# Performance work log

Hardware: AMD Instinct MI355X
Metric: run time of the kernel (lower is better)

## Reference

```python
import jax, jax.numpy as jnp
import numpy as np

DIM = 192
HEADS = 6
WS = 8
SHIFT = 4
POS_DIM = 12  # (dim//4)//4
HIDDEN = 768
EPS = 1e-5


def _win_partition(x, ws):
    B, H, W, C = x.shape
    x = x.reshape(B, H // ws, ws, W // ws, ws, C)
    return x.transpose(0, 1, 3, 2, 4, 5).reshape(-1, ws, ws, C)


def _win_reverse(w, ws, H, W):
    B = w.shape[0] // ((H // ws) * (W // ws))
    x = w.reshape(B, H // ws, W // ws, ws, ws, -1)
    return x.transpose(0, 1, 3, 2, 4, 5).reshape(B, H, W, -1)


def _calc_mask(H, W, ws, shift):
    img = np.zeros((1, H, W, 1), np.float32)
    sl = (slice(0, -ws), slice(-ws, -shift), slice(-shift, None))
    cnt = 0
    for hs in sl:
        for wsl in sl:
            img[:, hs, wsl, :] = cnt
            cnt += 1
    mw = img.reshape(1, H // ws, ws, W // ws, ws, 1).transpose(0, 1, 3, 2, 4, 5).reshape(-1, ws * ws)
    am = mw[:, None, :] - mw[:, :, None]
    am = np.where(am != 0, -100.0, 0.0).astype(np.float32)
    return am  # [nW, N, N]


def _rel_index(ws):
    coords = np.stack(np.meshgrid(np.arange(ws), np.arange(ws), indexing='ij')).reshape(2, -1)
    rel = (coords[:, :, None] - coords[:, None, :]).transpose(1, 2, 0)
    rel[..., 0] += ws - 1
    rel[..., 1] += ws - 1
    rel[..., 0] *= 2 * ws - 1
    return rel.sum(-1)  # [N, N]


def _biases(ws):
    bh = np.arange(1 - ws, ws)
    bw = np.arange(1 - ws, ws)
    b = np.stack(np.meshgrid(bh, bw, indexing='ij')).reshape(2, -1).T
    return b.astype(np.float32)  # [(2ws-1)^2, 2]


def _ln(x, g, b):
    mu = jnp.mean(x, -1, keepdims=True)
    var = jnp.var(x, -1, keepdims=True)
    return (x - mu) / jnp.sqrt(var + EPS) * g + b


def setup_inputs() -> dict:
    key = jax.random.key(0)
    ks = jax.random.split(key, 20)
    B, L, C = 8, 128 * 128, DIM
    d = {
        'x': jax.random.normal(ks[0], (B, L, C), jnp.float32),
        'k_v': jnp.zeros((1,), jnp.float32),
        'H': 128, 'W': 128,
        'n1_g': jnp.ones((C,)), 'n1_b': jnp.zeros((C,)),
        'qkv_w': jax.random.normal(ks[1], (C, 3 * C)) * 0.02,
        'qkv_b': jnp.zeros((3 * C,)),
        'proj_w': jax.random.normal(ks[2], (C, C)) * 0.02,
        'proj_b': jnp.zeros((C,)),
        'pp_w': jax.random.normal(ks[3], (2, POS_DIM)) * 0.02,
        'pp_b': jnp.zeros((POS_DIM,)),
        'p1_g': jnp.ones((POS_DIM,)), 'p1_b': jnp.zeros((POS_DIM,)),
        'p1_w': jax.random.normal(ks[4], (POS_DIM, POS_DIM)) * 0.02,
        'p1_bias': jnp.zeros((POS_DIM,)),
        'p2_g': jnp.ones((POS_DIM,)), 'p2_b': jnp.zeros((POS_DIM,)),
        'p2_w': jax.random.normal(ks[5], (POS_DIM, POS_DIM)) * 0.02,
        'p2_bias': jnp.zeros((POS_DIM,)),
        'p3_g': jnp.ones((POS_DIM,)), 'p3_b': jnp.zeros((POS_DIM,)),
        'p3_w': jax.random.normal(ks[6], (POS_DIM, HEADS)) * 0.02,
        'p3_bias': jnp.zeros((HEADS,)),
        'n2_g': jnp.ones((C,)), 'n2_b': jnp.zeros((C,)),
        'fc1_w': jax.random.normal(ks[7], (C, HIDDEN)) * 0.02,
        'fc1_b': jnp.zeros((HIDDEN,)),
        'fc2_w': jax.random.normal(ks[8], (HIDDEN, C)) * 0.02,
        'fc2_b': jnp.zeros((C,)),
    }
    return d


def reference(x, k_v, H, W, n1_g, n1_b, qkv_w, qkv_b, proj_w, proj_b,
              pp_w, pp_b, p1_g, p1_b, p1_w, p1_bias, p2_g, p2_b, p2_w, p2_bias,
              p3_g, p3_b, p3_w, p3_bias, n2_g, n2_b, fc1_w, fc1_b, fc2_w, fc2_b):
    B, L, C = x.shape
    N = WS * WS
    hd = C // HEADS
    scale = hd ** (-0.5)

    rel_idx = jnp.asarray(_rel_index(WS).reshape(-1))            # [N*N]
    biases = jnp.asarray(_biases(WS))                            # [(2WS-1)^2, 2]
    mask = jnp.asarray(_calc_mask(H, W, WS, SHIFT))              # [nW, N, N]

    shortcut = x
    h = _ln(x, n1_g, n1_b).reshape(B, H, W, C)
    h = jnp.roll(h, (-SHIFT, -SHIFT), (1, 2))
    xw = _win_partition(h, WS).reshape(-1, N, C)                 # [B*nW, N, C]
    B_ = xw.shape[0]

    qkv = (xw @ qkv_w + qkv_b).reshape(B_, N, 3, HEADS, hd).transpose(2, 0, 3, 1, 4)
    q, k, v = qkv[0] * scale, qkv[1], qkv[2]                     # [B_, H, N, hd]
    attn = jnp.einsum('bhnd,bhmd->bhnm', q, k)

    # dynamic position bias MLP (residual=False path)
    pos = biases @ pp_w + pp_b
    pos = jax.nn.relu(_ln(pos, p1_g, p1_b)) @ p1_w + p1_bias
    pos = jax.nn.relu(_ln(pos, p2_g, p2_b)) @ p2_w + p2_bias
    pos = jax.nn.relu(_ln(pos, p3_g, p3_b)) @ p3_w + p3_bias     # [(2WS-1)^2, HEADS]
    rpb = pos[rel_idx].reshape(N, N, HEADS).transpose(2, 0, 1)   # [HEADS, N, N]
    attn = attn + rpb[None]

    nW = mask.shape[0]
    attn = attn.reshape(B_ // nW, nW, HEADS, N, N) + mask[None, :, None]
    attn = jax.nn.softmax(attn.reshape(-1, HEADS, N, N), axis=-1)

    out = jnp.einsum('bhnm,bhmd->bhnd', attn, v).transpose(0, 2, 1, 3).reshape(B_, N, C)
    out = out @ proj_w + proj_b

    out = _win_reverse(out.reshape(-1, WS, WS, C), WS, H, W)
    out = jnp.roll(out, (SHIFT, SHIFT), (1, 2)).reshape(B, L, C)

    y = shortcut + out
    m = _ln(y, n2_g, n2_b)
    m = jax.nn.gelu(m @ fc1_w + fc1_b, approximate=False) @ fc2_w + fc2_b
    return y + m
```

## Files before the change

kernel.cpp:

```cpp
#include <hip/hip_runtime.h>
#include <hip/hip_bf16.h>
#include <math.h>

using bf16 = __hip_bfloat16;

typedef __bf16 bf16x8 __attribute__((ext_vector_type(8)));
typedef float f32x4 __attribute__((ext_vector_type(4)));

__device__ __forceinline__ float bf2f(bf16 v) { return __bfloat162float(v); }
__device__ __forceinline__ bf16 f2bf(float v) { return __float2bfloat16(v); }
__device__ __forceinline__ float nz(float v) { return (v == v) ? v : 0.0f; }

__device__ __forceinline__ void gload_lds16(const void* g, void* l) {
    __builtin_amdgcn_global_load_lds(
        (const __attribute__((address_space(1))) unsigned int*)g,
        (__attribute__((address_space(3))) unsigned int*)l, 16, 0, 0);
}

#define CDIM 192
#define NHEADS 6
#define ROWS 131072
#define HIDDEN 768

__global__ __launch_bounds__(256) void k_ln1_part(const float* __restrict__ x,
                                                  const float* __restrict__ g,
                                                  const float* __restrict__ bta,
                                                  bf16* __restrict__ xw) {
    int tid = threadIdx.x;
    int lane = tid & 63;
    int t = (blockIdx.x << 2) + (tid >> 6);
    int w = t >> 6, n = t & 63;
    int bb = w >> 8, wy = (w >> 4) & 15, wx = w & 15;
    int iy = n >> 3, ix = n & 7;
    int hs = (wy * 8 + iy + 4) & 127;
    int vs = (wx * 8 + ix + 4) & 127;
    const float* xr = x + ((size_t)bb * 16384 + (size_t)hs * 128 + vs) * CDIM;
    float v0 = nz(xr[lane]);
    float v1 = nz(xr[lane + 64]);
    float v2 = nz(xr[lane + 128]);
    float s = v0 + v1 + v2;
    float q = v0 * v0 + v1 * v1 + v2 * v2;
#pragma unroll
    for (int o = 32; o > 0; o >>= 1) { s += __shfl_xor(s, o); q += __shfl_xor(q, o); }
    float mean = s * (1.0f / 192.0f);
    float var = q * (1.0f / 192.0f) - mean * mean;
    float rs = rsqrtf(var + 1e-5f);
    bf16* orow = xw + (size_t)t * CDIM;
    orow[lane]       = f2bf((v0 - mean) * rs * g[lane]       + bta[lane]);
    orow[lane + 64]  = f2bf((v1 - mean) * rs * g[lane + 64]  + bta[lane + 64]);
    orow[lane + 128] = f2bf((v2 - mean) * rs * g[lane + 128] + bta[lane + 128]);
}

__global__ void k_transpose(const float* __restrict__ in, bf16* __restrict__ out, int K, int N) {
    int i = blockIdx.x * 256 + threadIdx.x;
    if (i < K * N) {
        int k = i / N, n = i - k * N;
        out[(size_t)n * K + k] = f2bf(in[i]);
    }
}

__global__ __launch_bounds__(256) void k_posmlp(
    const float* __restrict__ pp_w, const float* __restrict__ pp_b,
    const float* __restrict__ p1_g, const float* __restrict__ p1_b,
    const float* __restrict__ p1_w, const float* __restrict__ p1_bias,
    const float* __restrict__ p2_g, const float* __restrict__ p2_b,
    const float* __restrict__ p2_w, const float* __restrict__ p2_bias,
    const float* __restrict__ p3_g, const float* __restrict__ p3_b,
    const float* __restrict__ p3_w, const float* __restrict__ p3_bias,
    float* __restrict__ pos) {
    int i = threadIdx.x;
    if (i >= 225) return;
    float bh = (float)(i / 15 - 7), bw = (float)(i % 15 - 7);
    float v[12], u[12];
#pragma unroll
    for (int j = 0; j < 12; j++)
        v[j] = bh * pp_w[j] + bw * pp_w[12 + j] + pp_b[j];

    auto stage = [&](const float* gg, const float* bb2, const float* Wm, const float* bs, int OD) {
        float mean = 0.f;
        for (int j = 0; j < 12; j++) mean += v[j];
        mean *= (1.0f / 12.0f);
        float var = 0.f;
        for (int j = 0; j < 12; j++) { float d = v[j] - mean; var += d * d; }
        var *= (1.0f / 12.0f);
        float rs = rsqrtf(var + 1e-5f);
        for (int j = 0; j < 12; j++)
            u[j] = fmaxf((v[j] - mean) * rs * gg[j] + bb2[j], 0.0f);
        for (int o = 0; o < OD; o++) {
            float a = bs[o];
            for (int j = 0; j < 12; j++) a += u[j] * Wm[j * OD + o];
            v[o] = a;
        }
    };
    stage(p1_g, p1_b, p1_w, p1_bias, 12);
    stage(p2_g, p2_b, p2_w, p2_bias, 12);
    stage(p3_g, p3_b, p3_w, p3_bias, 6);
    for (int h = 0; h < 6; h++) pos[i * 6 + h] = v[h];
}

template <int EPI, typename OutT>
__global__ __launch_bounds__(256) void k_gemm(const bf16* __restrict__ A,
                                              const bf16* __restrict__ Bt,
                                              const float* __restrict__ bias,
                                              OutT* __restrict__ Cd,
                                              int M, int N, int K,
                                              const float* __restrict__ xres,
                                              const float* __restrict__ g2,
                                              const float* __restrict__ b2,
                                              float* __restrict__ yout,
                                              bf16* __restrict__ h2out) {
    constexpr int BM = 128, BN = 192, BK = 64;
    __shared__ __align__(16) unsigned short As[2][BM * BK];
    __shared__ __align__(16) unsigned short Bs[2][BN * BK];
    int tid = threadIdx.x;
    int wv = tid >> 6, lane = tid & 63;
    int lm = lane & 15, quad = lane >> 4;
    int sub = lane >> 3;
    int cb8 = (((lane & 7) ^ sub) << 3);
    int n0 = blockIdx.x * BN;
    int m0 = blockIdx.y * BM;

    const bf16* aSrc = A  + (size_t)(m0 + wv * 32 + sub) * K + cb8;
    const bf16* bSrc = Bt + (size_t)(n0 + wv * 48 + sub) * K + cb8;

    auto stage = [&](int buf, int k0) {
#pragma unroll
        for (int i = 0; i < 4; ++i)
            gload_lds16(aSrc + (size_t)(i * 8) * K + k0,
                        &As[buf][(wv * 32 + i * 8) * 64]);
#pragma unroll
        for (int i = 0; i < 6; ++i)
            gload_lds16(bSrc + (size_t)(i * 8) * K + k0,
                        &Bs[buf][(wv * 48 + i * 8) * 64]);
    };

    f32x4 acc[2][12] = {};

    auto compute = [&](int buf) {
#pragma unroll
        for (int ks = 0; ks < BK; ks += 32) {
            int xk = (ks + quad * 8) ^ ((lm & 7) << 3);
            bf16x8 af[2];
#pragma unroll
            for (int im = 0; im < 2; ++im)
                af[im] = *(const bf16x8*)&As[buf][(wv * 32 + im * 16 + lm) * 64 + xk];
#pragma unroll
            for (int in = 0; in < 12; ++in) {
                bf16x8 bq = *(const bf16x8*)&Bs[buf][(in * 16 + lm) * 64 + xk];
#pragma unroll
                for (int im = 0; im < 2; ++im)
                    acc[im][in] = __builtin_amdgcn_mfma_f32_16x16x32_bf16(
                        af[im], bq, acc[im][in], 0, 0, 0);
            }
        }
    };

    const int nt = K / BK;
    stage(0, 0);
    stage(1, BK);
    int cur = 0;
    for (int t = 0; t < nt; ++t) {
        if (t + 1 < nt)
            asm volatile("s_waitcnt vmcnt(10)" ::: "memory");
        else
            asm volatile("s_waitcnt vmcnt(0)" ::: "memory");
        __builtin_amdgcn_s_barrier();
        compute(cur);
        if (t + 2 < nt) {
            __builtin_amdgcn_s_barrier();
            stage(cur, (t + 2) * BK);
        }
        cur ^= 1;
    }

    if (EPI == 0 || EPI == 1) {
#pragma unroll
        for (int im = 0; im < 2; ++im) {
            int rbase = m0 + wv * 32 + im * 16 + quad * 4;
#pragma unroll
            for (int in = 0; in < 12; ++in) {
                int cg = n0 + in * 16 + lm;
                float bv = bias[cg];
#pragma unroll
                for (int r = 0; r < 4; ++r) {
                    float v = acc[im][in][r] + bv;
                    if (EPI == 1) v = 0.5f * v * (1.0f + erff(v * 0.70710678118654752f));
                    Cd[(size_t)(rbase + r) * N + cg] = (OutT)v;
                }
            }
        }
    } else if (EPI == 2) {
#pragma unroll
        for (int im = 0; im < 2; ++im) {
            int rbase = m0 + wv * 32 + im * 16 + quad * 4;
#pragma unroll
            for (int in = 0; in < 12; ++in) {
                int cg = in * 16 + lm;
                float bv = bias[cg];
#pragma unroll
                for (int r = 0; r < 4; ++r) {
                    size_t o = (size_t)(rbase + r) * 192 + cg;
                    yout[o] = acc[im][in][r] + bv + yout[o];
                }
            }
        }
    } else {
#pragma unroll
        for (int im = 0; im < 2; ++im) {
            int rbase = m0 + wv * 32 + im * 16 + quad * 4;
#pragma unroll
            for (int r = 0; r < 4; ++r) {
                int grow = rbase + r;
                int w = grow >> 6, n = grow & 63;
                int bb = w >> 8, wy = (w >> 4) & 15, wx = w & 15;
                int iy = n >> 3, ix = n & 7;
                int hs = (wy * 8 + iy + 4) & 127;
                int vs = (wx * 8 + ix + 4) & 127;
                size_t xrow = ((size_t)bb * 16384 + (size_t)hs * 128 + vs) * 192;
                float vv[12];
                float s = 0.f, q = 0.f;
#pragma unroll
                for (int in = 0; in < 12; ++in) {
                    int col = in * 16 + lm;
                    float v = acc[im][in][r] + bias[col] + nz(xres[xrow + col]);
                    yout[xrow + col] = v;
                    vv[in] = v; s += v; q += v * v;
                }
#pragma unroll
                for (int o = 1; o < 16; o <<= 1) {
                    s += __shfl_xor(s, o); q += __shfl_xor(q, o);
                }
                float mean = s * (1.0f / 192.0f);
                float var = q * (1.0f / 192.0f) - mean * mean;
                float rsv = rsqrtf(var + 1e-5f);
#pragma unroll
                for (int in = 0; in < 12; ++in) {
                    int col = in * 16 + lm;
                    h2out[xrow + col] = f2bf((vv[in] - mean) * rsv * g2[col] + b2[col]);
                }
            }
        }
    }
}

__global__ __launch_bounds__(256) void k_attn(const bf16* __restrict__ qkv,
                                              const float* __restrict__ pos,
                                              bf16* __restrict__ outp) {
    __shared__ __align__(16) unsigned short Qs[64 * 40];
    __shared__ __align__(16) unsigned short Ks[64 * 40];
    __shared__ __align__(16) unsigned short Vt[32 * 72];
    __shared__ __align__(16) unsigned short Ps[64 * 72];
    int w = blockIdx.x, tid = threadIdx.x;
    int wv = tid >> 6, lane = tid & 63;
    int lm = lane & 15, quad = lane >> 4;
    int wy = (w >> 4) & 15, wx = w & 15;
    bool edge = (wy == 15) || (wx == 15);
    const float scale = 0.17677669529663687f;

    int srow = tid >> 2, scol = (tid & 3) << 3;
    const unsigned short* gq =
        (const unsigned short*)qkv + ((size_t)w * 64 + srow) * 576 + scol;

    int nbase = wv * 16 + quad * 4;

    for (int h = 0; h < 6; ++h) {
        uint4 uq = *(const uint4*)(gq + h * 32);
        uint4 uk = *(const uint4*)(gq + h * 32 + 192);
        uint4 uv = *(const uint4*)(gq + h * 32 + 384);
        *(uint4*)&Qs[srow * 40 + scol] = uq;
        *(uint4*)&Ks[srow * 40 + scol] = uk;
        const unsigned short* pv = (const unsigned short*)&uv;
#pragma unroll
        for (int j = 0; j < 8; j++) Vt[(scol + j) * 72 + srow] = pv[j];
        __syncthreads();

        f32x4 acc[4];
        bf16x8 af = *(const bf16x8*)&Qs[(wv * 16 + lm) * 40 + quad * 8];
#pragma unroll
        for (int ct = 0; ct < 4; ++ct) {
            bf16x8 bfk = *(const bf16x8*)&Ks[(ct * 16 + lm) * 40 + quad * 8];
            f32x4 z = {0.f, 0.f, 0.f, 0.f};
            acc[ct] = __builtin_amdgcn_mfma_f32_16x16x32_bf16(af, bfk, z, 0, 0, 0);
        }

        float sv[4][4];
#pragma unroll
        for (int ct = 0; ct < 4; ++ct) {
            int m = ct * 16 + lm;
            int iym = m >> 3, ixm = m & 7;
            int hm = wy * 8 + iym, wm = wx * 8 + ixm;
            int ridm = (hm < 120 ? 0 : (hm < 124 ? 1 : 2)) * 3 +
                       (wm < 120 ? 0 : (wm < 124 ? 1 : 2));
#pragma unroll
            for (int r = 0; r < 4; r++) {
                int n = nbase + r;
                int iyn = n >> 3, ixn = n & 7;
                float s = acc[ct][r] * scale +
                          pos[((iyn - iym + 7) * 15 + (ixn - ixm + 7)) * 6 + h];
                if (edge) {
                    int hn = wy * 8 + iyn, wn = wx * 8 + ixn;
                    int ridn = (hn < 120 ? 0 : (hn < 124 ? 1 : 2)) * 3 +
                               (wn < 120 ? 0 : (wn < 124 ? 1 : 2));
                    if (ridn != ridm) s -= 100.0f;
                }
                sv[ct][r] = s;
            }
        }

#pragma unroll
        for (int r = 0; r < 4; r++) {
            float mx = fmaxf(fmaxf(sv[0][r], sv[1][r]), fmaxf(sv[2][r], sv[3][r]));
#pragma unroll
            for (int o = 1; o < 16; o <<= 1) mx = fmaxf(mx, __shfl_xor(mx, o));
            float e0 = expf(sv[0][r] - mx), e1 = expf(sv[1][r] - mx);
            float e2 = expf(sv[2][r] - mx), e3 = expf(sv[3][r] - mx);
            float sum = e0 + e1 + e2 + e3;
#pragma unroll
            for (int o = 1; o < 16; o <<= 1) sum += __shfl_xor(sum, o);
            float inv = 1.0f / sum;
            int n = nbase + r;
            *(bf16*)&Ps[n * 72 + lm]      = f2bf(e0 * inv);
            *(bf16*)&Ps[n * 72 + 16 + lm] = f2bf(e1 * inv);
            *(bf16*)&Ps[n * 72 + 32 + lm] = f2bf(e2 * inv);
            *(bf16*)&Ps[n * 72 + 48 + lm] = f2bf(e3 * inv);
        }
        __syncthreads();

        f32x4 o0 = {0.f, 0.f, 0.f, 0.f}, o1 = {0.f, 0.f, 0.f, 0.f};
#pragma unroll
        for (int kc = 0; kc < 2; kc++) {
            bf16x8 pa = *(const bf16x8*)&Ps[(wv * 16 + lm) * 72 + kc * 32 + quad * 8];
            bf16x8 vb0 = *(const bf16x8*)&Vt[lm * 72 + kc * 32 + quad * 8];
            bf16x8 vb1 = *(const bf16x8*)&Vt[(16 + lm) * 72 + kc * 32 + quad * 8];
            o0 = __builtin_amdgcn_mfma_f32_16x16x32_bf16(pa, vb0, o0, 0, 0, 0);
            o1 = __builtin_amdgcn_mfma_f32_16x16x32_bf16(pa, vb1, o1, 0, 0, 0);
        }
#pragma unroll
        for (int r = 0; r < 4; r++) {
            int n = nbase + r;
            size_t base = ((size_t)w * 64 + n) * 192 + h * 32;
            outp[base + lm]      = f2bf(o0[r]);
            outp[base + 16 + lm] = f2bf(o1[r]);
        }
        __syncthreads();
    }
}

extern "C" void kernel_launch(void* const* d_in, const int* in_sizes, int n_in,
                              void* d_out, int out_size, void* d_ws, size_t ws_size,
                              hipStream_t stream) {
    (void)in_sizes; (void)n_in; (void)out_size;
    const float* x      = (const float*)d_in[0];
    const float* n1_g   = (const float*)d_in[4];
    const float* n1_b   = (const float*)d_in[5];
    const float* qkv_w  = (const float*)d_in[6];
    const float* qkv_b  = (const float*)d_in[7];
    const float* proj_w = (const float*)d_in[8];
    const float* proj_b = (const float*)d_in[9];
    const float* pp_w   = (const float*)d_in[10];
    const float* pp_b   = (const float*)d_in[11];
    const float* p1_g   = (const float*)d_in[12];
    const float* p1_b   = (const float*)d_in[13];
    const float* p1_w   = (const float*)d_in[14];
    const float* p1_bias= (const float*)d_in[15];
    const float* p2_g   = (const float*)d_in[16];
    const float* p2_b   = (const float*)d_in[17];
    const float* p2_w   = (const float*)d_in[18];
    const float* p2_bias= (const float*)d_in[19];
    const float* p3_g   = (const float*)d_in[20];
    const float* p3_b   = (const float*)d_in[21];
    const float* p3_w   = (const float*)d_in[22];
    const float* p3_bias= (const float*)d_in[23];
    const float* n2_g   = (const float*)d_in[24];
    const float* n2_b   = (const float*)d_in[25];
    const float* fc1_w  = (const float*)d_in[26];
    const float* fc1_b  = (const float*)d_in[27];
    const float* fc2_w  = (const float*)d_in[28];
    const float* fc2_b  = (const float*)d_in[29];

    char* ws = (char*)d_ws;
    size_t off = 0;
    auto alloc = [&](size_t bytes) -> char* {
        char* p = ws + off;
        off += (bytes + 255) & ~(size_t)255;
        return p;
    };
    bf16* qkvwT  = (bf16*)alloc((size_t)CDIM * 576 * 2);
    bf16* projwT = (bf16*)alloc((size_t)CDIM * CDIM * 2);
    bf16* fc1wT  = (bf16*)alloc((size_t)CDIM * HIDDEN * 2);
    bf16* fc2wT  = (bf16*)alloc((size_t)HIDDEN * CDIM * 2);
    float* pos   = (float*)alloc(225 * 6 * 4);

    const size_t flatNeed = (size_t)ROWS * CDIM * 2
                          + (size_t)ROWS * HIDDEN * 2
                          + (size_t)ROWS * CDIM * 2
                          + (1u << 20);
    const bool flat = (ws_size > off) && ((ws_size - off) >= flatNeed);
    const int NCH = flat ? 1 : 8;
    const int NIMG = flat ? 8 : 1;
    const size_t R = (size_t)16384 * NIMG;

    bf16 *xw_b, *qkv_buf, *attn_b, *h2_b, *fc1_buf;
    if (flat) {
        bf16* region0 = (bf16*)alloc((size_t)ROWS * CDIM * 2);
        bf16* region1 = (bf16*)alloc((size_t)ROWS * HIDDEN * 2);
        h2_b = (bf16*)alloc((size_t)ROWS * CDIM * 2);
        xw_b = attn_b = region0;
        qkv_buf = region1;
        fc1_buf = region1;
    } else {
        xw_b     = (bf16*)alloc(R * CDIM * 2);
        qkv_buf  = (bf16*)alloc(R * 576 * 2);
        attn_b   = (bf16*)alloc(R * CDIM * 2);
        h2_b     = (bf16*)alloc(R * CDIM * 2);
        fc1_buf  = (bf16*)alloc(R * HIDDEN * 2);
    }
    float* yout = (float*)d_out;

    k_transpose<<<(CDIM * 576 + 255) / 256, 256, 0, stream>>>(qkv_w, qkvwT, CDIM, 576);
    k_transpose<<<(CDIM * CDIM + 255) / 256, 256, 0, stream>>>(proj_w, projwT, CDIM, CDIM);
    k_transpose<<<(CDIM * HIDDEN + 255) / 256, 256, 0, stream>>>(fc1_w, fc1wT, CDIM, HIDDEN);
    k_transpose<<<(HIDDEN * CDIM + 255) / 256, 256, 0, stream>>>(fc2_w, fc2wT, HIDDEN, CDIM);
    k_posmlp<<<1, 256, 0, stream>>>(pp_w, pp_b, p1_g, p1_b, p1_w, p1_bias,
                                    p2_g, p2_b, p2_w, p2_bias,
                                    p3_g, p3_b, p3_w, p3_bias, pos);

    for (int c = 0; c < NCH; ++c) {
        const float* x_c = x + (size_t)c * 16384 * CDIM;
        float* y_c = yout + (size_t)c * 16384 * CDIM;

        k_ln1_part<<<(int)(R / 4), 256, 0, stream>>>(x_c, n1_g, n1_b, xw_b);

        k_gemm<0, bf16><<<dim3(576 / 192, (int)(R / 128)), 256, 0, stream>>>(
            xw_b, qkvwT, qkv_b, qkv_buf, (int)R, 576, CDIM,
            nullptr, nullptr, nullptr, nullptr, nullptr);

        k_attn<<<(int)(R / 64), 256, 0, stream>>>(qkv_buf, pos, attn_b);

        k_gemm<3, bf16><<<dim3(1, (int)(R / 128)), 256, 0, stream>>>(
            attn_b, projwT, proj_b, (bf16*)nullptr, (int)R, CDIM, CDIM,
            x_c, n2_g, n2_b, y_c, h2_b);

        k_gemm<1, bf16><<<dim3(HIDDEN / 192, (int)(R / 128)), 256, 0, stream>>>(
            h2_b, fc1wT, fc1_b, fc1_buf, (int)R, HIDDEN, CDIM,
            nullptr, nullptr, nullptr, nullptr, nullptr);

        k_gemm<2, float><<<dim3(1, (int)(R / 128)), 256, 0, stream>>>(
            fc1_buf, fc2wT, fc2_b, y_c, (int)R, CDIM, HIDDEN,
            nullptr, nullptr, nullptr, y_c, nullptr);
    }
}
```

Before: 677.4 us.

## Fuse fc1, GELU and fc2 into one MLP kernel with LDS-resident hidden

```diff
diff --git a/kernel.cpp b/kernel.cpp
--- a/kernel.cpp
+++ b/kernel.cpp
@@ -15,6 +15,11 @@
     __builtin_amdgcn_global_load_lds(
         (const __attribute__((address_space(1))) unsigned int*)g,
         (__attribute__((address_space(3))) unsigned int*)l, 16, 0, 0);
+}
+
+__device__ __forceinline__ float fgelu(float v) {
+    float z = v * (1.5957691f + 0.07135481f * v * v);
+    return v / (1.0f + __expf(-z));
 }
 
 #define CDIM 192
@@ -173,7 +178,7 @@
         cur ^= 1;
     }
 
-    if (EPI == 0 || EPI == 1) {
+    if (EPI == 0) {
 #pragma unroll
         for (int im = 0; im < 2; ++im) {
             int rbase = m0 + wv * 32 + im * 16 + quad * 4;
@@ -184,23 +189,7 @@
 #pragma unroll
                 for (int r = 0; r < 4; ++r) {
                     float v = acc[im][in][r] + bv;
-                    if (EPI == 1) v = 0.5f * v * (1.0f + erff(v * 0.70710678118654752f));
                     Cd[(size_t)(rbase + r) * N + cg] = (OutT)v;
-                }
-            }
-        }
-    } else if (EPI == 2) {
-#pragma unroll
-        for (int im = 0; im < 2; ++im) {
-            int rbase = m0 + wv * 32 + im * 16 + quad * 4;
-#pragma unroll
-            for (int in = 0; in < 12; ++in) {
-                int cg = in * 16 + lm;
-                float bv = bias[cg];
-#pragma unroll
-                for (int r = 0; r < 4; ++r) {
-                    size_t o = (size_t)(rbase + r) * 192 + cg;
-                    yout[o] = acc[im][in][r] + bv + yout[o];
                 }
             }
         }
@@ -239,6 +228,115 @@
                     h2out[xrow + col] = f2bf((vv[in] - mean) * rsv * g2[col] + b2[col]);
                 }
             }
+        }
+    }
+}
+
+__global__ __launch_bounds__(512) void k_mlp(const bf16* __restrict__ h2,
+                                             const bf16* __restrict__ w1t,
+                                             const float* __restrict__ b1,
+                                             const bf16* __restrict__ w2t,
+                                             const float* __restrict__ b2,
+                                             float* __restrict__ y,
+                                             int M) {
+    __shared__ __align__(16) unsigned short Ah[3 * 128 * 64];
+    __shared__ __align__(16) unsigned short Bb[2][192 * 64];
+    __shared__ __align__(16) unsigned short Ps[3 * 128 * 64];
+    __shared__ float b1s[HIDDEN];
+    int tid = threadIdx.x;
+    int wv = tid >> 6, lane = tid & 63;
+    int lm = lane & 15, quad = lane >> 4;
+    int sub = lane >> 3;
+    int cb8 = (((lane & 7) ^ sub) << 3);
+    int m0 = blockIdx.x * 128;
+
+    for (int i = tid; i < HIDDEN; i += 512) b1s[i] = b1[i];
+
+#pragma unroll
+    for (int i = 0; i < 6; ++i) {
+        int j = wv * 6 + i;
+        int p = j >> 4, r0 = (j & 15) * 8;
+        gload_lds16(h2 + (size_t)(m0 + r0 + sub) * 192 + p * 64 + cb8,
+                    &Ah[p * 8192 + r0 * 64]);
+    }
+
+    auto stageChunk = [&](int c) {
+        int kb = c / 6, ph = c % 6, slot = c & 1;
+        if (ph < 3) {
+            const bf16* s = w1t + (size_t)(kb * 192 + wv * 24 + sub) * 192 + ph * 64 + cb8;
+#pragma unroll
+            for (int i = 0; i < 3; ++i)
+                gload_lds16(s + (size_t)(i * 8) * 192, &Bb[slot][(wv * 24 + i * 8) * 64]);
+        } else {
+            const bf16* s = w2t + (size_t)(wv * 24 + sub) * 768 + kb * 192 + (ph - 3) * 64 + cb8;
+#pragma unroll
+            for (int i = 0; i < 3; ++i)
+                gload_lds16(s + (size_t)(i * 8) * 768, &Bb[slot][(wv * 24 + i * 8) * 64]);
+        }
+    };
+
+    f32x4 a1[12];
+    f32x4 a2[12] = {};
+
+    auto docompute = [&](const unsigned short* Ap, int slot, f32x4 (&acc)[12]) {
+#pragma unroll
+        for (int ks = 0; ks < 64; ks += 32) {
+            int xk = (ks + quad * 8) ^ ((lm & 7) << 3);
+            bf16x8 af = *(const bf16x8*)&Ap[(wv * 16 + lm) * 64 + xk];
+#pragma unroll
+            for (int in = 0; in < 12; ++in) {
+                bf16x8 bq = *(const bf16x8*)&Bb[slot][(in * 16 + lm) * 64 + xk];
+                acc[in] = __builtin_amdgcn_mfma_f32_16x16x32_bf16(af, bq, acc[in], 0, 0, 0);
+            }
+        }
+    };
+
+    stageChunk(0);
+    stageChunk(1);
+    asm volatile("s_waitcnt lgkmcnt(0)" ::: "memory");
+
+    for (int c = 0; c < 24; ++c) {
+        if (c < 22)
+            asm volatile("s_waitcnt vmcnt(3)" ::: "memory");
+        else
+            asm volatile("s_waitcnt vmcnt(0)" ::: "memory");
+        __builtin_amdgcn_s_barrier();
+        int kb = c / 6, ph = c % 6, slot = c & 1;
+        if (ph == 0) {
+#pragma unroll
+            for (int in = 0; in < 12; ++in) a1[in] = (f32x4){0.f, 0.f, 0.f, 0.f};
+        }
+        if (ph < 3)
+            docompute(&Ah[ph * 8192], slot, a1);
+        else
+            docompute(&Ps[(ph - 3) * 8192], slot, a2);
+        __builtin_amdgcn_s_barrier();
+        if (c + 2 < 24) stageChunk(c + 2);
+        if (ph == 2) {
+#pragma unroll
+            for (int in = 0; in < 12; ++in) {
+                int col = in * 16 + lm;
+                float bv = b1s[kb * 192 + col];
+                int plane = col >> 6, c6 = col & 63;
+#pragma unroll
+                for (int r = 0; r < 4; ++r) {
+                    int rl = wv * 16 + quad * 4 + r;
+                    float ge = fgelu(a1[in][r] + bv);
+                    int sc = ((((c6 >> 3) ^ (rl & 7)) << 3) | (col & 7));
+                    *(bf16*)&Ps[plane * 8192 + rl * 64 + sc] = f2bf(ge);
+                }
+            }
+        }
+    }
+
+#pragma unroll
+    for (int in = 0; in < 12; ++in) {
+        int col = in * 16 + lm;
+        float bv = b2[col];
+#pragma unroll
+        for (int r = 0; r < 4; ++r) {
+            size_t o = (size_t)(m0 + wv * 16 + quad * 4 + r) * 192 + col;
+            y[o] = a2[in][r] + bv + y[o];
         }
     }
 }
@@ -400,20 +498,18 @@
     const int NIMG = flat ? 8 : 1;
     const size_t R = (size_t)16384 * NIMG;
 
-    bf16 *xw_b, *qkv_buf, *attn_b, *h2_b, *fc1_buf;
+    bf16 *xw_b, *qkv_buf, *attn_b, *h2_b;
     if (flat) {
         bf16* region0 = (bf16*)alloc((size_t)ROWS * CDIM * 2);
         bf16* region1 = (bf16*)alloc((size_t)ROWS * HIDDEN * 2);
         h2_b = (bf16*)alloc((size_t)ROWS * CDIM * 2);
         xw_b = attn_b = region0;
         qkv_buf = region1;
-        fc1_buf = region1;
     } else {
         xw_b     = (bf16*)alloc(R * CDIM * 2);
         qkv_buf  = (bf16*)alloc(R * 576 * 2);
         attn_b   = (bf16*)alloc(R * CDIM * 2);
         h2_b     = (bf16*)alloc(R * CDIM * 2);
-        fc1_buf  = (bf16*)alloc(R * HIDDEN * 2);
     }
     float* yout = (float*)d_out;
 
@@ -441,12 +537,7 @@
             attn_b, projwT, proj_b, (bf16*)nullptr, (int)R, CDIM, CDIM,
             x_c, n2_g, n2_b, y_c, h2_b);
 
-        k_gemm<1, bf16><<<dim3(HIDDEN / 192, (int)(R / 128)), 256, 0, stream>>>(
-            h2_b, fc1wT, fc1_b, fc1_buf, (int)R, HIDDEN, CDIM,
-            nullptr, nullptr, nullptr, nullptr, nullptr);
-
-        k_gemm<2, float><<<dim3(1, (int)(R / 128)), 256, 0, stream>>>(
-            fc1_buf, fc2wT, fc2_b, y_c, (int)R, CDIM, HIDDEN,
-            nullptr, nullptr, nullptr, y_c, nullptr);
-    }
-}
+        k_mlp<<<(int)(R / 128), 512, 0, stream>>>(
+            h2_b, fc1wT, fc1_b, fc2wT, fc2_b, y_c, (int)R);
+    }
+}
```

Measured after the change: 646.2 us. 1.05x faster.
